# Kernel tuning notes

Hardware: AMD Instinct MI355X
Metric: run time of the kernel (lower is better)

The kernel has to match this reference:

```python
import jax, jax.numpy as jnp
import numpy as np

B, T, C, NH = 8, 1024, 1024, 16
DH = C // NH  # 64


def setup_inputs() -> dict:
    key = jax.random.key(0)
    ks = jax.random.split(key, 7)
    s = 1.0 / np.sqrt(C)
    return {
        "x": jax.random.normal(ks[0], (B, T, C), dtype=jnp.float32),
        "Wq": jax.random.normal(ks[1], (C, C), dtype=jnp.float32) * s,
        "bq": jnp.zeros((C,), dtype=jnp.float32),
        "Wk": jax.random.normal(ks[2], (C, C), dtype=jnp.float32) * s,
        "bk": jnp.zeros((C,), dtype=jnp.float32),
        "Wv": jax.random.normal(ks[3], (C, C), dtype=jnp.float32) * s,
        "bv": jnp.zeros((C,), dtype=jnp.float32),
    }


def reference(x, Wq, bq, Wk, bk, Wv, bv):
    # Linear projections (weights stored as [in, out])
    q = x @ Wq + bq  # [B, T, C]
    k = x @ Wk + bk
    v = x @ Wv + bv
    q = q.reshape(B, T, NH, DH)
    k = k.reshape(B, T, NH, DH)
    v = v.reshape(B, T, NH, DH)
    scale = 1.0 / np.sqrt(DH)
    # NOTE: source module's causal mask buffer is all-ones due to a non-inplace
    # masked_fill bug, so attention is NON-causal (mask multiply is a no-op).
    attn = jnp.einsum("bqhd,bkhd->bhqk", q, k) * scale  # [B, NH, T, T]
    attn = jax.nn.softmax(attn, axis=-1)
    # dropout is identity (p=0 / eval)
    o = jnp.einsum("bhqk,bkhd->bqhd", attn, v)  # [B, T, NH, DH]
    return o.reshape(B, T, C)
```

## Files before the change

### kernel.cpp

```cpp
#include <hip/hip_runtime.h>


#define B_  8
#define T_  1024
#define C_  1024
#define NH_ 16
#define DH_ 64
#define M_  (B_ * T_)

typedef __bf16 bf16x8 __attribute__((ext_vector_type(8)));
typedef float  floatx4 __attribute__((ext_vector_type(4)));

__device__ __forceinline__ unsigned short f2bf(float f) {
    unsigned int u = __float_as_uint(f);
    unsigned int r = (u + 0x7fffu + ((u >> 16) & 1u)) >> 16;
    return (unsigned short)r;
}

__device__ __forceinline__ void gload_lds16(const void* g, void* l) {
    __builtin_amdgcn_global_load_lds(
        (const __attribute__((address_space(1))) unsigned int*)g,
        (__attribute__((address_space(3))) unsigned int*)l, 16, 0, 0);
}

__global__ __launch_bounds__(256) void cast_x_kernel(
    const float* __restrict__ x, unsigned short* __restrict__ xb, int n4)
{
    int i = blockIdx.x * 256 + threadIdx.x;
    if (i < n4) {
        float4 v = ((const float4*)x)[i];
        ushort4 o;
        o.x = f2bf(v.x); o.y = f2bf(v.y); o.z = f2bf(v.z); o.w = f2bf(v.w);
        ((ushort4*)xb)[i] = o;
    }
}

__global__ __launch_bounds__(256) void transpose_w_kernel(
    const float* __restrict__ Wq, const float* __restrict__ Wk,
    const float* __restrict__ Wv, unsigned short* __restrict__ WtAll)
{
    int which = blockIdx.y;
    const float* W = (which == 0) ? Wq : ((which == 1) ? Wk : Wv);
    unsigned short* out = WtAll + (size_t)which * C_ * C_;

    __shared__ __align__(16) unsigned short tile[64 * 65];
    int tb = blockIdx.x;
    int k0 = (tb >> 4) * 64, n0 = (tb & 15) * 64;
    int c = threadIdx.x & 63, r0 = threadIdx.x >> 6;

    for (int j = 0; j < 16; ++j) {
        int r = r0 + j * 4;
        tile[c * 65 + r] = f2bf(W[(size_t)(k0 + r) * C_ + n0 + c]);
    }
    __syncthreads();
    for (int j = 0; j < 16; ++j) {
        int r = r0 + j * 4;
        out[(size_t)(n0 + r) * C_ + k0 + c] = tile[r * 65 + c];
    }
}

__global__ __launch_bounds__(256) void qkv_gemm_kernel(
    const unsigned short* __restrict__ xb,
    const unsigned short* __restrict__ WtAll,
    const float* __restrict__ bq, const float* __restrict__ bk,
    const float* __restrict__ bv,
    unsigned short* __restrict__ Qb, unsigned short* __restrict__ Kb,
    unsigned short* __restrict__ Vt)
{
    int which = blockIdx.z;
    const unsigned short* W = WtAll + (size_t)which * C_ * C_;
    const float* bias = (which == 0) ? bq : ((which == 1) ? bk : bv);
    unsigned short* outp = (which == 0) ? Qb : ((which == 1) ? Kb : Vt);
    float oscale = (which == 0) ? 0.125f * 1.44269504f : 1.0f;

    __shared__ __align__(16) unsigned short As[128 * 64];
    __shared__ __align__(16) unsigned short Bs[128 * 64];

    int tid = threadIdx.x;
    int wave = tid >> 6, lane = tid & 63;
    int quad = lane >> 4, l16 = lane & 15, l7 = l16 & 7;
    int wm = wave >> 1, wn = wave & 1;
    int bm = blockIdx.x, bn = blockIdx.y;

    floatx4 acc[4][4] = {};

    for (int kk = 0; kk < C_; kk += 64) {
        __syncthreads();
        #pragma unroll
        for (int i = 0; i < 4; ++i) {
            int c = (wave * 4 + i) * 64 + lane;
            int row = c >> 3;
            int lcol = ((c & 7) ^ (row & 7)) * 8;
            gload_lds16(&xb[(size_t)(bm * 128 + row) * C_ + kk + lcol],
                        &As[(wave * 4 + i) * 512]);
            gload_lds16(&W[(size_t)(bn * 128 + row) * C_ + kk + lcol],
                        &Bs[(wave * 4 + i) * 512]);
        }
        __syncthreads();
        #pragma unroll
        for (int s = 0; s < 2; ++s) {
            bf16x8 a[4], bfr[4];
            #pragma unroll
            for (int mt = 0; mt < 4; ++mt) {
                int row = wm * 64 + mt * 16 + l16;
                a[mt] = *(const bf16x8*)&As[row * 64 + (((s * 4 + quad)) ^ l7) * 8];
            }
            #pragma unroll
            for (int nt = 0; nt < 4; ++nt) {
                int row = wn * 64 + nt * 16 + l16;
                bfr[nt] = *(const bf16x8*)&Bs[row * 64 + (((s * 4 + quad)) ^ l7) * 8];
            }
            #pragma unroll
            for (int mt = 0; mt < 4; ++mt)
                #pragma unroll
                for (int nt = 0; nt < 4; ++nt)
                    acc[mt][nt] = __builtin_amdgcn_mfma_f32_16x16x32_bf16(
                        a[mt], bfr[nt], acc[mt][nt], 0, 0, 0);
        }
    }

    #pragma unroll
    for (int nt = 0; nt < 4; ++nt) {
        int colg = bn * 128 + wn * 64 + nt * 16 + l16;
        int h = colg >> 6, d = colg & 63;
        float bval = bias[colg];
        #pragma unroll
        for (int mt = 0; mt < 4; ++mt) {
            #pragma unroll
            for (int reg = 0; reg < 4; ++reg) {
                int rowg = bm * 128 + wm * 64 + mt * 16 + quad * 4 + reg;
                int bb = rowg >> 10, t = rowg & (T_ - 1);
                float val = (acc[mt][nt][reg] + bval) * oscale;
                size_t idx;
                if (which < 2)
                    idx = ((size_t)(bb * NH_ + h) * T_ + t) * DH_ + d;
                else
                    idx = ((size_t)(bb * NH_ + h) * DH_ + d) * T_ + t;
                outp[idx] = f2bf(val);
            }
        }
    }
}

__global__ __launch_bounds__(256) void attn_kernel(
    const unsigned short* __restrict__ Qb,
    const unsigned short* __restrict__ Kb,
    const unsigned short* __restrict__ Vt,
    float* __restrict__ out)
{
    int bh = blockIdx.x;
    int qblk = blockIdx.y;
    int b = bh >> 4, h = bh & (NH_ - 1);
    int tid = threadIdx.x;
    int wave = tid >> 6, lane = tid & 63;
    int quad = lane >> 4, l16 = lane & 15, l7 = l16 & 7;

    const unsigned short* Qh = Qb + (size_t)bh * T_ * DH_;
    const unsigned short* Kh = Kb + (size_t)bh * T_ * DH_;
    const unsigned short* Vh = Vt + (size_t)bh * DH_ * T_;

    __shared__ __align__(16) unsigned short Ks[64 * 64];
    __shared__ __align__(16) unsigned short Vs[64 * 64];
    __shared__ __align__(16) unsigned short Ps[4][2][16 * 72];

    bf16x8 qa[2][2];
    #pragma unroll
    for (int mt = 0; mt < 2; ++mt) {
        int qrow = qblk * 128 + (wave * 2 + mt) * 16 + l16;
        qa[mt][0] = *(const bf16x8*)&Qh[(size_t)qrow * DH_ + quad * 8];
        qa[mt][1] = *(const bf16x8*)&Qh[(size_t)qrow * DH_ + 32 + quad * 8];
    }

    floatx4 o_acc[2][4] = {};
    float l_i[2] = {0.0f, 0.0f};

    for (int kt = 0; kt < T_ / 64; ++kt) {
        __syncthreads();
        #pragma unroll
        for (int i = 0; i < 2; ++i) {
            int c = (wave * 2 + i) * 64 + lane;
            int row = c >> 3;
            int lcol = ((c & 7) ^ (row & 7)) * 8;
            gload_lds16(&Kh[(size_t)(kt * 64 + row) * DH_ + lcol],
                        &Ks[(wave * 2 + i) * 512]);
            gload_lds16(&Vh[(size_t)row * T_ + kt * 64 + lcol],
                        &Vs[(wave * 2 + i) * 512]);
        }
        __syncthreads();

        floatx4 st[2][4] = {};
        #pragma unroll
        for (int nt = 0; nt < 4; ++nt) {
            int r = (nt * 16 + l16) * 64;
            bf16x8 k0 = *(const bf16x8*)&Ks[r + ((quad    ) ^ l7) * 8];
            bf16x8 k1 = *(const bf16x8*)&Ks[r + ((quad + 4) ^ l7) * 8];
            #pragma unroll
            for (int mt = 0; mt < 2; ++mt) {
                st[mt][nt] = __builtin_amdgcn_mfma_f32_16x16x32_bf16(k0, qa[mt][0], st[mt][nt], 0, 0, 0);
                st[mt][nt] = __builtin_amdgcn_mfma_f32_16x16x32_bf16(k1, qa[mt][1], st[mt][nt], 0, 0, 0);
            }
        }

        #pragma unroll
        for (int mt = 0; mt < 2; ++mt) {
            float rs = 0.0f;
            #pragma unroll
            for (int nt = 0; nt < 4; ++nt) {
                float e0 = exp2f(st[mt][nt][0]);
                float e1 = exp2f(st[mt][nt][1]);
                float e2 = exp2f(st[mt][nt][2]);
                float e3 = exp2f(st[mt][nt][3]);
                rs += (e0 + e1) + (e2 + e3);
                ushort4 pk;
                pk.x = f2bf(e0); pk.y = f2bf(e1); pk.z = f2bf(e2); pk.w = f2bf(e3);
                *(ushort4*)&Ps[wave][mt][l16 * 72 + nt * 16 + quad * 4] = pk;
            }
            rs += __shfl_xor(rs, 16);
            rs += __shfl_xor(rs, 32);
            l_i[mt] += rs;
        }

        #pragma unroll
        for (int s2 = 0; s2 < 2; ++s2) {
            bf16x8 vb[4];
            #pragma unroll
            for (int dt = 0; dt < 4; ++dt)
                vb[dt] = *(const bf16x8*)&Vs[(dt * 16 + l16) * 64 + ((s2 * 4 + quad) ^ l7) * 8];
            #pragma unroll
            for (int mt = 0; mt < 2; ++mt) {
                bf16x8 pb = *(const bf16x8*)&Ps[wave][mt][l16 * 72 + s2 * 32 + quad * 8];
                #pragma unroll
                for (int dt = 0; dt < 4; ++dt)
                    o_acc[mt][dt] = __builtin_amdgcn_mfma_f32_16x16x32_bf16(
                        vb[dt], pb, o_acc[mt][dt], 0, 0, 0);
            }
        }
    }

    #pragma unroll
    for (int mt = 0; mt < 2; ++mt) {
        float inv = 1.0f / l_i[mt];
        int t = qblk * 128 + (wave * 2 + mt) * 16 + l16;
        float* op = &out[((size_t)b * T_ + t) * C_ + h * DH_];
        #pragma unroll
        for (int dt = 0; dt < 4; ++dt) {
            float4 v;
            v.x = o_acc[mt][dt][0] * inv;
            v.y = o_acc[mt][dt][1] * inv;
            v.z = o_acc[mt][dt][2] * inv;
            v.w = o_acc[mt][dt][3] * inv;
            *(float4*)&op[dt * 16 + quad * 4] = v;
        }
    }
}

extern "C" void kernel_launch(void* const* d_in, const int* in_sizes, int n_in,
                              void* d_out, int out_size, void* d_ws, size_t ws_size,
                              hipStream_t stream) {
    const float* x  = (const float*)d_in[0];
    const float* Wq = (const float*)d_in[1];
    const float* bq = (const float*)d_in[2];
    const float* Wk = (const float*)d_in[3];
    const float* bk = (const float*)d_in[4];
    const float* Wv = (const float*)d_in[5];
    const float* bv = (const float*)d_in[6];
    float* out = (float*)d_out;

    char* ws = (char*)d_ws;
    size_t off = 0;
    unsigned short* xb = (unsigned short*)(ws + off); off += (size_t)M_ * C_ * 2;
    unsigned short* Wt = (unsigned short*)(ws + off); off += (size_t)3 * C_ * C_ * 2;
    unsigned short* Qb = (unsigned short*)(ws + off); off += (size_t)M_ * C_ * 2;
    unsigned short* Kb = (unsigned short*)(ws + off); off += (size_t)M_ * C_ * 2;
    unsigned short* Vt = (unsigned short*)(ws + off); off += (size_t)M_ * C_ * 2;

    int n4 = (M_ * C_) / 4;
    cast_x_kernel<<<dim3(n4 / 256), dim3(256), 0, stream>>>(x, xb, n4);

    transpose_w_kernel<<<dim3(256, 3), dim3(256), 0, stream>>>(Wq, Wk, Wv, Wt);

    qkv_gemm_kernel<<<dim3(M_ / 128, C_ / 128, 3), dim3(256), 0, stream>>>(
        xb, Wt, bq, bk, bv, Qb, Kb, Vt);

    attn_kernel<<<dim3(B_ * NH_, T_ / 128), dim3(256), 0, stream>>>(Qb, Kb, Vt, out);
}
```

Measured before the change: 244.9 us.

## Merge prep kernels, vectorize QKV epilogue stores, double attention KV tile

Folds the x cast and the weight transpose into one prep kernel to save a launch. The QKV GEMM swaps MFMA operand order for Q/K so each lane holds contiguous d values, letting it write packed 4-element bf16 stores; V keeps contiguous t values and also uses packed stores. The attention kernel loads 128 keys per iteration instead of 64, halving the barrier count, with a wider XOR swizzle for V. The larger K/V tiles raise LDS use, which may reduce occupancy.

```diff
diff --git a/kernel.cpp b/kernel.cpp
--- a/kernel.cpp
+++ b/kernel.cpp
@@ -17,34 +17,46 @@
     return (unsigned short)r;
 }
 
+__device__ __forceinline__ unsigned int f2bf2(float a, float b) {
+    unsigned int ua = __float_as_uint(a), ub = __float_as_uint(b);
+    ua += 0x7fffu + ((ua >> 16) & 1u);
+    ub += 0x7fffu + ((ub >> 16) & 1u);
+#if __has_builtin(__builtin_amdgcn_perm)
+    return __builtin_amdgcn_perm(ub, ua, 0x07060302u);
+#else
+    return (ua >> 16) | (ub & 0xffff0000u);
+#endif
+}
+
 __device__ __forceinline__ void gload_lds16(const void* g, void* l) {
     __builtin_amdgcn_global_load_lds(
         (const __attribute__((address_space(1))) unsigned int*)g,
         (__attribute__((address_space(3))) unsigned int*)l, 16, 0, 0);
 }
 
-__global__ __launch_bounds__(256) void cast_x_kernel(
-    const float* __restrict__ x, unsigned short* __restrict__ xb, int n4)
-{
-    int i = blockIdx.x * 256 + threadIdx.x;
-    if (i < n4) {
-        float4 v = ((const float4*)x)[i];
-        ushort4 o;
-        o.x = f2bf(v.x); o.y = f2bf(v.y); o.z = f2bf(v.z); o.w = f2bf(v.w);
-        ((ushort4*)xb)[i] = o;
-    }
-}
-
-__global__ __launch_bounds__(256) void transpose_w_kernel(
+__global__ __launch_bounds__(256) void prep_kernel(
+    const float* __restrict__ x, unsigned short* __restrict__ xb,
     const float* __restrict__ Wq, const float* __restrict__ Wk,
     const float* __restrict__ Wv, unsigned short* __restrict__ WtAll)
 {
-    int which = blockIdx.y;
+    int blk = blockIdx.x;
+    if (blk < 8192) {
+        int i = blk * 256 + threadIdx.x;
+        float4 v = ((const float4*)x)[i];
+        ushort4 o;
+        unsigned int lo = f2bf2(v.x, v.y), hi = f2bf2(v.z, v.w);
+        o.x = (unsigned short)lo; o.y = (unsigned short)(lo >> 16);
+        o.z = (unsigned short)hi; o.w = (unsigned short)(hi >> 16);
+        ((ushort4*)xb)[i] = o;
+        return;
+    }
+    int tb3 = blk - 8192;
+    int which = tb3 >> 8;
+    int tb = tb3 & 255;
     const float* W = (which == 0) ? Wq : ((which == 1) ? Wk : Wv);
     unsigned short* out = WtAll + (size_t)which * C_ * C_;
 
     __shared__ __align__(16) unsigned short tile[64 * 65];
-    int tb = blockIdx.x;
     int k0 = (tb >> 4) * 64, n0 = (tb & 15) * 64;
     int c = threadIdx.x & 63, r0 = threadIdx.x >> 6;
 
@@ -70,7 +82,6 @@
     int which = blockIdx.z;
     const unsigned short* W = WtAll + (size_t)which * C_ * C_;
     const float* bias = (which == 0) ? bq : ((which == 1) ? bk : bv);
-    unsigned short* outp = (which == 0) ? Qb : ((which == 1) ? Kb : Vt);
     float oscale = (which == 0) ? 0.125f * 1.44269504f : 1.0f;
 
     __shared__ __align__(16) unsigned short As[128 * 64];
@@ -103,40 +114,64 @@
             #pragma unroll
             for (int mt = 0; mt < 4; ++mt) {
                 int row = wm * 64 + mt * 16 + l16;
-                a[mt] = *(const bf16x8*)&As[row * 64 + (((s * 4 + quad)) ^ l7) * 8];
+                a[mt] = *(const bf16x8*)&As[row * 64 + ((s * 4 + quad) ^ l7) * 8];
             }
             #pragma unroll
             for (int nt = 0; nt < 4; ++nt) {
                 int row = wn * 64 + nt * 16 + l16;
-                bfr[nt] = *(const bf16x8*)&Bs[row * 64 + (((s * 4 + quad)) ^ l7) * 8];
-            }
-            #pragma unroll
-            for (int mt = 0; mt < 4; ++mt)
-                #pragma unroll
-                for (int nt = 0; nt < 4; ++nt)
-                    acc[mt][nt] = __builtin_amdgcn_mfma_f32_16x16x32_bf16(
-                        a[mt], bfr[nt], acc[mt][nt], 0, 0, 0);
-        }
-    }
-
-    #pragma unroll
-    for (int nt = 0; nt < 4; ++nt) {
-        int colg = bn * 128 + wn * 64 + nt * 16 + l16;
-        int h = colg >> 6, d = colg & 63;
-        float bval = bias[colg];
+                bfr[nt] = *(const bf16x8*)&Bs[row * 64 + ((s * 4 + quad) ^ l7) * 8];
+            }
+            if (which < 2) {
+                #pragma unroll
+                for (int mt = 0; mt < 4; ++mt)
+                    #pragma unroll
+                    for (int nt = 0; nt < 4; ++nt)
+                        acc[mt][nt] = __builtin_amdgcn_mfma_f32_16x16x32_bf16(
+                            bfr[nt], a[mt], acc[mt][nt], 0, 0, 0);
+            } else {
+                #pragma unroll
+                for (int mt = 0; mt < 4; ++mt)
+                    #pragma unroll
+                    for (int nt = 0; nt < 4; ++nt)
+                        acc[mt][nt] = __builtin_amdgcn_mfma_f32_16x16x32_bf16(
+                            a[mt], bfr[nt], acc[mt][nt], 0, 0, 0);
+            }
+        }
+    }
+
+    if (which < 2) {
+        unsigned short* outp = (which == 0) ? Qb : Kb;
         #pragma unroll
         for (int mt = 0; mt < 4; ++mt) {
-            #pragma unroll
-            for (int reg = 0; reg < 4; ++reg) {
-                int rowg = bm * 128 + wm * 64 + mt * 16 + quad * 4 + reg;
-                int bb = rowg >> 10, t = rowg & (T_ - 1);
-                float val = (acc[mt][nt][reg] + bval) * oscale;
-                size_t idx;
-                if (which < 2)
-                    idx = ((size_t)(bb * NH_ + h) * T_ + t) * DH_ + d;
-                else
-                    idx = ((size_t)(bb * NH_ + h) * DH_ + d) * T_ + t;
-                outp[idx] = f2bf(val);
+            int tg = bm * 128 + wm * 64 + mt * 16 + l16;
+            int bb = tg >> 10, t = tg & (T_ - 1);
+            #pragma unroll
+            for (int nt = 0; nt < 4; ++nt) {
+                int colg = bn * 128 + wn * 64 + nt * 16 + quad * 4;
+                int h = colg >> 6, d = colg & 63;
+                float4 b4 = *(const float4*)&bias[colg];
+                uint2 o;
+                o.x = f2bf2((acc[mt][nt][0] + b4.x) * oscale,
+                            (acc[mt][nt][1] + b4.y) * oscale);
+                o.y = f2bf2((acc[mt][nt][2] + b4.z) * oscale,
+                            (acc[mt][nt][3] + b4.w) * oscale);
+                *(uint2*)&outp[((size_t)(bb * NH_ + h) * T_ + t) * DH_ + d] = o;
+            }
+        }
+    } else {
+        #pragma unroll
+        for (int nt = 0; nt < 4; ++nt) {
+            int colg = bn * 128 + wn * 64 + nt * 16 + l16;
+            int h = colg >> 6, d = colg & 63;
+            float bval = bias[colg];
+            #pragma unroll
+            for (int mt = 0; mt < 4; ++mt) {
+                int tg = bm * 128 + wm * 64 + mt * 16 + quad * 4;
+                int bb = tg >> 10, t = tg & (T_ - 1);
+                uint2 o;
+                o.x = f2bf2(acc[mt][nt][0] + bval, acc[mt][nt][1] + bval);
+                o.y = f2bf2(acc[mt][nt][2] + bval, acc[mt][nt][3] + bval);
+                *(uint2*)&Vt[((size_t)(bb * NH_ + h) * DH_ + d) * T_ + t] = o;
             }
         }
     }
@@ -159,8 +194,8 @@
     const unsigned short* Kh = Kb + (size_t)bh * T_ * DH_;
     const unsigned short* Vh = Vt + (size_t)bh * DH_ * T_;
 
-    __shared__ __align__(16) unsigned short Ks[64 * 64];
-    __shared__ __align__(16) unsigned short Vs[64 * 64];
+    __shared__ __align__(16) unsigned short Ks[128 * 64];
+    __shared__ __align__(16) unsigned short Vs[64 * 128];
     __shared__ __align__(16) unsigned short Ps[4][2][16 * 72];
 
     bf16x8 qa[2][2];
@@ -174,65 +209,73 @@
     floatx4 o_acc[2][4] = {};
     float l_i[2] = {0.0f, 0.0f};
 
-    for (int kt = 0; kt < T_ / 64; ++kt) {
+    for (int kt2 = 0; kt2 < T_ / 128; ++kt2) {
         __syncthreads();
         #pragma unroll
-        for (int i = 0; i < 2; ++i) {
-            int c = (wave * 2 + i) * 64 + lane;
-            int row = c >> 3;
-            int lcol = ((c & 7) ^ (row & 7)) * 8;
-            gload_lds16(&Kh[(size_t)(kt * 64 + row) * DH_ + lcol],
-                        &Ks[(wave * 2 + i) * 512]);
-            gload_lds16(&Vh[(size_t)row * T_ + kt * 64 + lcol],
-                        &Vs[(wave * 2 + i) * 512]);
+        for (int i = 0; i < 4; ++i) {
+            int c = (wave * 4 + i) * 64 + lane;
+            int krow = c >> 3;
+            int klcol = ((c & 7) ^ (krow & 7)) * 8;
+            gload_lds16(&Kh[(size_t)(kt2 * 128 + krow) * DH_ + klcol],
+                        &Ks[(wave * 4 + i) * 512]);
+            int vrow = c >> 4;
+            int vlcol = (((c & 15) ^ (vrow & 15))) * 8;
+            gload_lds16(&Vh[(size_t)vrow * T_ + kt2 * 128 + vlcol],
+                        &Vs[(wave * 4 + i) * 512]);
         }
         __syncthreads();
 
-        floatx4 st[2][4] = {};
-        #pragma unroll
-        for (int nt = 0; nt < 4; ++nt) {
-            int r = (nt * 16 + l16) * 64;
-            bf16x8 k0 = *(const bf16x8*)&Ks[r + ((quad    ) ^ l7) * 8];
-            bf16x8 k1 = *(const bf16x8*)&Ks[r + ((quad + 4) ^ l7) * 8];
+        #pragma unroll
+        for (int kh = 0; kh < 2; ++kh) {
+            floatx4 st[2][4] = {};
+            #pragma unroll
+            for (int nt = 0; nt < 4; ++nt) {
+                int r = (kh * 64 + nt * 16 + l16) * 64;
+                bf16x8 k0 = *(const bf16x8*)&Ks[r + ((quad    ) ^ l7) * 8];
+                bf16x8 k1 = *(const bf16x8*)&Ks[r + ((quad + 4) ^ l7) * 8];
+                #pragma unroll
+                for (int mt = 0; mt < 2; ++mt) {
+                    st[mt][nt] = __builtin_amdgcn_mfma_f32_16x16x32_bf16(k0, qa[mt][0], st[mt][nt], 0, 0, 0);
+                    st[mt][nt] = __builtin_amdgcn_mfma_f32_16x16x32_bf16(k1, qa[mt][1], st[mt][nt], 0, 0, 0);
+                }
+            }
+
             #pragma unroll
             for (int mt = 0; mt < 2; ++mt) {
-                st[mt][nt] = __builtin_amdgcn_mfma_f32_16x16x32_bf16(k0, qa[mt][0], st[mt][nt], 0, 0, 0);
-                st[mt][nt] = __builtin_amdgcn_mfma_f32_16x16x32_bf16(k1, qa[mt][1], st[mt][nt], 0, 0, 0);
-            }
-        }
-
-        #pragma unroll
-        for (int mt = 0; mt < 2; ++mt) {
-            float rs = 0.0f;
-            #pragma unroll
-            for (int nt = 0; nt < 4; ++nt) {
-                float e0 = exp2f(st[mt][nt][0]);
-                float e1 = exp2f(st[mt][nt][1]);
-                float e2 = exp2f(st[mt][nt][2]);
-                float e3 = exp2f(st[mt][nt][3]);
-                rs += (e0 + e1) + (e2 + e3);
-                ushort4 pk;
-                pk.x = f2bf(e0); pk.y = f2bf(e1); pk.z = f2bf(e2); pk.w = f2bf(e3);
-                *(ushort4*)&Ps[wave][mt][l16 * 72 + nt * 16 + quad * 4] = pk;
-            }
-            rs += __shfl_xor(rs, 16);
-            rs += __shfl_xor(rs, 32);
-            l_i[mt] += rs;
-        }
-
-        #pragma unroll
-        for (int s2 = 0; s2 < 2; ++s2) {
-            bf16x8 vb[4];
-            #pragma unroll
-            for (int dt = 0; dt < 4; ++dt)
-                vb[dt] = *(const bf16x8*)&Vs[(dt * 16 + l16) * 64 + ((s2 * 4 + quad) ^ l7) * 8];
-            #pragma unroll
-            for (int mt = 0; mt < 2; ++mt) {
-                bf16x8 pb = *(const bf16x8*)&Ps[wave][mt][l16 * 72 + s2 * 32 + quad * 8];
-                #pragma unroll
-                for (int dt = 0; dt < 4; ++dt)
-                    o_acc[mt][dt] = __builtin_amdgcn_mfma_f32_16x16x32_bf16(
-                        vb[dt], pb, o_acc[mt][dt], 0, 0, 0);
+                float rs = 0.0f;
+                #pragma unroll
+                for (int nt = 0; nt < 4; ++nt) {
+                    float e0 = exp2f(st[mt][nt][0]);
+                    float e1 = exp2f(st[mt][nt][1]);
+                    float e2 = exp2f(st[mt][nt][2]);
+                    float e3 = exp2f(st[mt][nt][3]);
+                    rs += (e0 + e1) + (e2 + e3);
+                    uint2 pk;
+                    pk.x = f2bf2(e0, e1);
+                    pk.y = f2bf2(e2, e3);
+                    *(uint2*)&Ps[wave][mt][l16 * 72 + nt * 16 + quad * 4] = pk;
+                }
+                rs += __shfl_xor(rs, 16);
+                rs += __shfl_xor(rs, 32);
+                l_i[mt] += rs;
+            }
+
+            #pragma unroll
+            for (int s2 = 0; s2 < 2; ++s2) {
+                bf16x8 vb[4];
+                #pragma unroll
+                for (int dt = 0; dt < 4; ++dt) {
+                    int chv = (kh * 8 + s2 * 4 + quad) ^ l16;
+                    vb[dt] = *(const bf16x8*)&Vs[(dt * 16 + l16) * 128 + chv * 8];
+                }
+                #pragma unroll
+                for (int mt = 0; mt < 2; ++mt) {
+                    bf16x8 pb = *(const bf16x8*)&Ps[wave][mt][l16 * 72 + s2 * 32 + quad * 8];
+                    #pragma unroll
+                    for (int dt = 0; dt < 4; ++dt)
+                        o_acc[mt][dt] = __builtin_amdgcn_mfma_f32_16x16x32_bf16(
+                            vb[dt], pb, o_acc[mt][dt], 0, 0, 0);
+                }
             }
         }
     }
@@ -274,10 +317,7 @@
     unsigned short* Kb = (unsigned short*)(ws + off); off += (size_t)M_ * C_ * 2;
     unsigned short* Vt = (unsigned short*)(ws + off); off += (size_t)M_ * C_ * 2;
 
-    int n4 = (M_ * C_) / 4;
-    cast_x_kernel<<<dim3(n4 / 256), dim3(256), 0, stream>>>(x, xb, n4);
-
-    transpose_w_kernel<<<dim3(256, 3), dim3(256), 0, stream>>>(Wq, Wk, Wv, Wt);
+    prep_kernel<<<dim3(8960), dim3(256), 0, stream>>>(x, xb, Wq, Wk, Wv, Wt);
 
     qkv_gemm_kernel<<<dim3(M_ / 128, C_ / 128, 3), dim3(256), 0, stream>>>(
         xb, Wt, bq, bk, bv, Qb, Kb, Vt);
```

Result: faster. 233.3 us (-4.7%).
